# Optimization experiments

Measured on AMD Instinct MI355X. Metric: run time of the kernel, lower is better.

Reference implementation:

```python
import jax, jax.numpy as jnp
import numpy as np

D_NUM, P_NUM, LAYER, EMB = 1500, 4500, 3, 128


def _xavier(k, shape):
    lim = float(np.sqrt(6.0 / (shape[0] + shape[1])))
    return jax.random.uniform(k, shape, minval=-lim, maxval=lim, dtype=jnp.float32)


def _sym_norm(adj):
    # D^{-1/2} A D^{-1/2}, zero-degree safe (utils._create_*_adj_mat)
    deg = adj.sum(axis=1)
    dinv = jnp.where(deg > 0, jax.lax.rsqrt(jnp.maximum(deg, 1e-12)), 0.0)
    return adj * dinv[:, None] * dinv[None, :]


def _gcn(adj, emb, num):
    # LightGCN-style propagation: mean of layer-0..num embeddings (utils._gcn)
    def step(e, _):
        e = adj @ e
        return e, e
    _, layers = jax.lax.scan(step, emb, None, length=num)
    return (emb + layers.sum(axis=0)) / (num + 1)


def _neighbor_mean(mat, feats):
    # vectorized form of the per-row python loop: mean of feats over j where mat[i,j]==1, zeros if no neighbor
    m = (mat == 1.0).astype(feats.dtype)
    cnt = m.sum(axis=1, keepdims=True)
    return jnp.where(cnt > 0, (m @ feats) / jnp.maximum(cnt, 1.0), 0.0)


def _get_weight(emb, WA, BA, HA):
    return jax.nn.log_softmax(jax.nn.relu(emb @ WA + BA) @ HA, axis=0)


def setup_inputs():
    k = jax.random.split(jax.random.key(0), 24)
    N = D_NUM + P_NUM
    A = (jax.random.uniform(k[0], (5, N, N)) < 0.005).astype(jnp.float32)
    z = lambda: jnp.zeros((EMB,), jnp.float32)
    h = lambda: jnp.full((EMB, 1), 0.01, jnp.float32)
    return {
        "A": A,
        "drug_structure": jax.random.normal(k[1], (D_NUM, 160), jnp.float32),
        "protein_structure": jax.random.normal(k[2], (P_NUM, 512), jnp.float32),
        "lin_drug_w": _xavier(k[3], (160, EMB)), "lin_drug_b": z(),
        "lin_pro_w": _xavier(k[4], (512, EMB)), "lin_pro_b": z(),
        "p_weight": _xavier(k[5], (EMB, EMB)),
        "d_weight_i": _xavier(k[6], (EMB, EMB)),
        "pd_weight_p": _xavier(k[7], (EMB, EMB)),
        "pd_weight_d": _xavier(k[8], (EMB, EMB)),
        "dp_weight_p": _xavier(k[9], (EMB, EMB)),
        "WA_drug": _xavier(k[10], (EMB, EMB)), "BA_drug": z(), "HA_drug": h(),
        "WB_drug": _xavier(k[11], (EMB, EMB)), "BB_drug": z(), "HB_drug": h(),
        "WA_pro": _xavier(k[12], (EMB, EMB)), "BA_pro": z(), "HA_pro": h(),
        "WB_pro": _xavier(k[13], (EMB, EMB)), "BB_pro": z(), "HB_pro": h(),
        "WA_sim": _xavier(k[14], (EMB, EMB)), "BA_sim": z(), "HA_sim": h(),
        "layer": LAYER,
    }


def reference(A, drug_structure, protein_structure, lin_drug_w, lin_drug_b, lin_pro_w, lin_pro_b,
              p_weight, d_weight_i, pd_weight_p, pd_weight_d, dp_weight_p,
              WA_drug, BA_drug, HA_drug, WB_drug, BB_drug, HB_drug,
              WA_pro, BA_pro, HA_pro, WB_pro, BB_pro, HB_pro,
              WA_sim, BA_sim, HA_sim, layer):
    D, P = D_NUM, P_NUM
    R = A[0, :D, D:D + P]                       # drug-protein relation [D,P]
    dru_str = drug_structure @ lin_drug_w + lin_drug_b      # [D,128]
    pro_str = protein_structure @ lin_pro_w + lin_pro_b     # [P,128]

    def rel_emb(mat, feats, w):
        nei = _neighbor_mean(mat, feats)
        adj = _sym_norm((mat == 1.0).astype(feats.dtype))
        return _gcn(adj, feats @ w, layer), nei

    dru_rel_emb, dru_rel_nei = rel_emb(A[2, :D, :D], dru_str, d_weight_i)
    pro_rel_emb, pro_rel_nei = rel_emb(A[3, D:, D:], pro_str, p_weight)
    dru_sim_emb, dru_sim_nei = rel_emb(A[4, :D, :D], dru_str, d_weight_i)

    dru_tem = _neighbor_mean(R, pro_rel_nei)    # [D,128]
    # NB: torch 'dru_rel_nei + dru_sim_nei' concatenates python LISTS, and only
    # indices < D are ever read, so pro_tem effectively uses dru_rel_nei only.
    pro_tem = _neighbor_mean(R.T, dru_rel_nei)  # [P,128]

    # bipartite symmetric-normalized adjacency [[0,R],[R^T,0]]
    bip = jnp.zeros((D + P, D + P), R.dtype)
    bip = bip.at[:D, D:].set(R).at[D:, :D].set(R.T)
    adj = _sym_norm(bip)

    one_all = 0.8 * dru_str + 0.2 * dru_tem
    two_all = 0.8 * pro_str + 0.2 * pro_tem
    one_emb = dru_str @ pd_weight_d
    two_all = (two_all @ dp_weight_p) @ pd_weight_d
    two_emb = pro_str @ pd_weight_p
    dru_int = _gcn(adj, jnp.concatenate([one_emb, two_all], axis=0), layer)[:D]
    pro_int = _gcn(adj, jnp.concatenate([one_all, two_emb], axis=0), layer)[D:]

    drug_w = _get_weight(dru_int, WA_drug, BA_drug, HA_drug)
    pro_w = _get_weight(pro_int, WA_pro, BA_pro, HA_pro)
    dru_rel_w = _get_weight(dru_rel_emb, WB_drug, BB_drug, HB_drug)
    pro_rel_w = _get_weight(pro_rel_emb, WB_pro, BB_pro, HB_pro)
    dru_sim_w = _get_weight(dru_sim_emb, WA_sim, BA_sim, HA_sim)

    # faithful to source (including its asymmetric renormalization); dropout is eval-mode identity
    a_w = drug_w / (drug_w + dru_rel_w + dru_sim_w)
    b_w = dru_rel_w / (a_w + dru_rel_w + dru_sim_w)
    c_w = 1.0 - a_w - b_w
    fin_dru = a_w * dru_int + b_w * dru_rel_emb + c_w * dru_sim_emb

    pa = pro_w / (pro_w + pro_rel_w)
    pb = 1.0 - pa
    fin_pro = pa * pro_int + pb * pro_rel_emb

    y = fin_dru @ fin_pro.T                     # [D,P]
    y = (y - y.mean()) / jnp.std(y, ddof=1)     # torch.std is unbiased
    return jax.nn.sigmoid(y)
```

## Files before the change

### kernel.cpp

```cpp
#include <hip/hip_runtime.h>
#include <hip/hip_bf16.h>

constexpr int CAP = 128;

__global__ void k_build(const float* __restrict__ M, long ldm, int rows, int cols,
                        int col_off,
                        int* __restrict__ idx, int* __restrict__ cnt,
                        float* __restrict__ invcnt, float* __restrict__ dinv)
{
    int row = blockIdx.x * 4 + (threadIdx.x >> 6);
    if (row >= rows) return;
    int lane = threadIdx.x & 63;
    const float* p = M + (long)row * ldm;
    int* ri = idx + (long)row * CAP;
    int base = 0;
    for (int j0 = 0; j0 < cols; j0 += 64) {
        int j = j0 + lane;
        bool hit = (j < cols) && (p[j] == 1.0f);
        unsigned long long m = __ballot(hit);
        if (hit) {
            int pos = base + (int)__popcll(m & ((1ULL << lane) - 1ULL));
            if (pos < CAP) ri[pos] = j + col_off;
        }
        base += (int)__popcll(m);
    }
    if (lane == 0) {
        cnt[row] = base < CAP ? base : CAP;
        invcnt[row] = (base > 0) ? 1.0f / (float)base : 0.0f;
        dinv[row]   = (base > 0) ? rsqrtf((float)base) : 0.0f;
    }
}

__global__ void k_scatter_T(int* __restrict__ idx, int* __restrict__ cnt, int topRows)
{
    int row = blockIdx.x * 4 + (threadIdx.x >> 6);
    if (row >= topRows) return;
    int lane = threadIdx.x & 63;
    int n = cnt[row];
    const int* ri = idx + (long)row * CAP;
    for (int k = lane; k < n; k += 64) {
        int j = ri[k];
        int pos = atomicAdd(&cnt[j], 1);
        if (pos < CAP) idx[(long)j * CAP + pos] = row;
    }
}

__global__ void k_invdeg(const int* __restrict__ cnt, int n,
                         float* __restrict__ invcnt, float* __restrict__ dinv)
{
    int i = blockIdx.x * 256 + threadIdx.x;
    if (i < n) {
        int c = cnt[i];
        invcnt[i] = (c > 0) ? 1.0f / (float)c : 0.0f;
        dinv[i]   = (c > 0) ? rsqrtf((float)c) : 0.0f;
    }
}

__global__ __launch_bounds__(256)
void k_spmm_sp(const int* __restrict__ idx, const int* __restrict__ cnt,
               int rows, int mod,
               const float* __restrict__ X,
               const float* __restrict__ rs, const float* __restrict__ cs,
               float* __restrict__ out, float* __restrict__ accp)
{
    int c = threadIdx.x & 127;
    int row = blockIdx.x * 2 + (threadIdx.x >> 7);
    if (row >= rows) return;
    int r_loc = row, xoff = 0;
    if (row >= mod) { r_loc = row - mod; xoff = mod; }
    int n = cnt[r_loc];
    const int* ri = idx + (long)r_loc * CAP;
    float acc = 0.0f;
    int k = 0;
    for (; k + 4 <= n; k += 4) {
        int j0 = ri[k], j1 = ri[k + 1], j2 = ri[k + 2], j3 = ri[k + 3];
        float x0 = X[(long)(j0 + xoff) * 128 + c];
        float x1 = X[(long)(j1 + xoff) * 128 + c];
        float x2 = X[(long)(j2 + xoff) * 128 + c];
        float x3 = X[(long)(j3 + xoff) * 128 + c];
        if (cs) { x0 *= cs[j0]; x1 *= cs[j1]; x2 *= cs[j2]; x3 *= cs[j3]; }
        acc += (x0 + x1) + (x2 + x3);
    }
    for (; k < n; ++k) {
        int j = ri[k];
        float x = X[(long)(j + xoff) * 128 + c];
        if (cs) x *= cs[j];
        acc += x;
    }
    float v = rs ? acc * rs[r_loc] : acc;
    long o = (long)row * 128 + c;
    out[o] = v;
    if (accp) accp[o] += v;
}

template<bool RELU>
__global__ __launch_bounds__(256)
void k_lin(const float* __restrict__ X, const float* __restrict__ X2,
           float pa, float pb, int rows, int K,
           const float* __restrict__ W, const float* __restrict__ bias,
           float* __restrict__ out, float* __restrict__ out2)
{
    __shared__ float Ws[64 * 128];
    int c  = threadIdx.x & 127;
    int row = blockIdx.x * 2 + (threadIdx.x >> 7);
    float acc = 0.0f;
    for (int k0 = 0; k0 < K; k0 += 64) {
        int chunk = min(64, K - k0);
        for (int e = threadIdx.x; e < chunk * 128; e += 256)
            Ws[e] = W[(long)(k0 + (e >> 7)) * 128 + (e & 127)];
        __syncthreads();
        if (row < rows) {
            const float* xr = X + (long)row * K + k0;
            const float* x2r = X2 ? X2 + (long)row * K + k0 : nullptr;
            #pragma unroll 4
            for (int kk = 0; kk < chunk; ++kk) {
                float v = xr[kk];
                if (X2) v = pa * v + pb * x2r[kk];
                acc += v * Ws[kk * 128 + c];
            }
        }
        __syncthreads();
    }
    if (row < rows) {
        float v = acc + (bias ? bias[c] : 0.0f);
        if (RELU) v = fmaxf(v, 0.0f);
        out[(long)row * 128 + c] = v;
        if (out2) out2[(long)row * 128 + c] = v;
    }
}

__global__ __launch_bounds__(256)
void k_attn(const float* __restrict__ X, int rows,
            const float* __restrict__ W, const float* __restrict__ B,
            const float* __restrict__ H, float* __restrict__ s)
{
    __shared__ float Ws[64 * 128];
    __shared__ float part[4];
    int c = threadIdx.x & 127;
    int row = blockIdx.x * 2 + (threadIdx.x >> 7);
    float acc = 0.0f;
    for (int k0 = 0; k0 < 128; k0 += 64) {
        for (int e = threadIdx.x; e < 64 * 128; e += 256)
            Ws[e] = W[(long)(k0 + (e >> 7)) * 128 + (e & 127)];
        __syncthreads();
        if (row < rows) {
            const float* xr = X + (long)row * 128 + k0;
            #pragma unroll 4
            for (int kk = 0; kk < 64; ++kk)
                acc += xr[kk] * Ws[kk * 128 + c];
        }
        __syncthreads();
    }
    float v = 0.0f;
    if (row < rows) v = fmaxf(acc + B[c], 0.0f) * H[c];
    for (int o = 32; o > 0; o >>= 1) v += __shfl_down(v, o, 64);
    if ((threadIdx.x & 63) == 0) part[threadIdx.x >> 6] = v;
    __syncthreads();
    if (threadIdx.x == 0 && row < rows)   s[row] = part[0] + part[1];
    if (threadIdx.x == 128 && row < rows) s[row] = part[2] + part[3];
}

__global__ void k_logsoftmax5(float* s0, int n0, float* s1, int n1,
                              float* s2, int n2, float* s3, int n3,
                              float* s4, int n4)
{
    float* s; int n;
    switch (blockIdx.x) {
        case 0: s = s0; n = n0; break;
        case 1: s = s1; n = n1; break;
        case 2: s = s2; n = n2; break;
        case 3: s = s3; n = n3; break;
        default: s = s4; n = n4; break;
    }
    __shared__ float red[256];
    int t = threadIdx.x;
    float m = -3.4e38f;
    for (int i = t; i < n; i += 256) m = fmaxf(m, s[i]);
    red[t] = m; __syncthreads();
    for (int o = 128; o > 0; o >>= 1) {
        if (t < o) red[t] = fmaxf(red[t], red[t + o]);
        __syncthreads();
    }
    m = red[0];
    __syncthreads();
    float sum = 0.0f;
    for (int i = t; i < n; i += 256) sum += expf(s[i] - m);
    red[t] = sum; __syncthreads();
    for (int o = 128; o > 0; o >>= 1) {
        if (t < o) red[t] += red[t + o];
        __syncthreads();
    }
    float lse = m + logf(red[0]);
    for (int i = t; i < n; i += 256) s[i] -= lse;
}

__global__ void k_scale(const float* __restrict__ src, float* __restrict__ dst,
                        long n, float sc)
{
    long i = (long)blockIdx.x * blockDim.x + threadIdx.x;
    if (i < n) dst[i] = src[i] * sc;
}

__global__ void k_axpby(const float* __restrict__ X, const float* __restrict__ Y,
                        float a, float b,
                        float* __restrict__ out, float* __restrict__ out2, long n)
{
    long i = (long)blockIdx.x * blockDim.x + threadIdx.x;
    if (i < n) {
        float v = a * X[i] + b * Y[i];
        out[i] = v;
        if (out2) out2[i] = v;
    }
}

__global__ void k_fin_dru(const float* __restrict__ wa, const float* __restrict__ wb,
                          const float* __restrict__ wc,
                          const float* __restrict__ ei, const float* __restrict__ er,
                          const float* __restrict__ es,
                          float* __restrict__ fin, int rows)
{
    long idx = (long)blockIdx.x * 256 + threadIdx.x;
    if (idx >= (long)rows * 128) return;
    int r = (int)(idx >> 7);
    float aL = wa[r], bL = wb[r], cL = wc[r];
    float a = aL / (aL + bL + cL);
    float b = bL / (a + bL + cL);
    float c = 1.0f - a - b;
    fin[idx] = a * ei[idx] + b * er[idx] + c * es[idx];
}

__global__ void k_fin_pro(const float* __restrict__ wa, const float* __restrict__ wb,
                          const float* __restrict__ ei, const float* __restrict__ er,
                          float* __restrict__ fin, int rows)
{
    long idx = (long)blockIdx.x * 256 + threadIdx.x;
    if (idx >= (long)rows * 128) return;
    int r = (int)(idx >> 7);
    float pa = wa[r] / (wa[r] + wb[r]);
    fin[idx] = pa * ei[idx] + (1.0f - pa) * er[idx];
}

__global__ void k_zero2(double* p)
{
    if (threadIdx.x < 2) p[threadIdx.x] = 0.0;
}

__global__ __launch_bounds__(256)
void k_ygemm(const float* __restrict__ Af, const float* __restrict__ Bf,
             int M, int N, float* __restrict__ y, double* __restrict__ stats)
{
    __shared__ float Ast[32][68];
    __shared__ float Bst[32][68];
    int i0 = blockIdx.y * 64, j0 = blockIdx.x * 64;
    int tx = threadIdx.x & 15, ty = threadIdx.x >> 4;
    float acc[4][4] = {};
    for (int k0 = 0; k0 < 128; k0 += 32) {
        for (int e = threadIdx.x; e < 64 * 32; e += 256) {
            int r = e >> 5, kk = e & 31;
            int ia = i0 + r, jb = j0 + r;
            Ast[kk][r] = (ia < M) ? Af[(long)ia * 128 + k0 + kk] : 0.0f;
            Bst[kk][r] = (jb < N) ? Bf[(long)jb * 128 + k0 + kk] : 0.0f;
        }
        __syncthreads();
        #pragma unroll 8
        for (int kk = 0; kk < 32; ++kk) {
            float a0 = Ast[kk][ty * 4 + 0], a1 = Ast[kk][ty * 4 + 1];
            float a2 = Ast[kk][ty * 4 + 2], a3 = Ast[kk][ty * 4 + 3];
            float b0 = Bst[kk][tx * 4 + 0], b1 = Bst[kk][tx * 4 + 1];
            float b2 = Bst[kk][tx * 4 + 2], b3 = Bst[kk][tx * 4 + 3];
            acc[0][0] += a0 * b0; acc[0][1] += a0 * b1; acc[0][2] += a0 * b2; acc[0][3] += a0 * b3;
            acc[1][0] += a1 * b0; acc[1][1] += a1 * b1; acc[1][2] += a1 * b2; acc[1][3] += a1 * b3;
            acc[2][0] += a2 * b0; acc[2][1] += a2 * b1; acc[2][2] += a2 * b2; acc[2][3] += a2 * b3;
            acc[3][0] += a3 * b0; acc[3][1] += a3 * b1; acc[3][2] += a3 * b2; acc[3][3] += a3 * b3;
        }
        __syncthreads();
    }
    double s1 = 0.0, s2 = 0.0;
    #pragma unroll
    for (int q = 0; q < 4; ++q) {
        int i = i0 + ty * 4 + q;
        if (i < M) {
            #pragma unroll
            for (int p = 0; p < 4; ++p) {
                int j = j0 + tx * 4 + p;
                if (j < N) {
                    float v = acc[q][p];
                    y[(long)i * N + j] = v;
                    s1 += v; s2 += (double)v * v;
                }
            }
        }
    }
    __shared__ double r1[256];
    __shared__ double r2[256];
    r1[threadIdx.x] = s1; r2[threadIdx.x] = s2;
    __syncthreads();
    for (int o = 128; o > 0; o >>= 1) {
        if (threadIdx.x < o) {
            r1[threadIdx.x] += r1[threadIdx.x + o];
            r2[threadIdx.x] += r2[threadIdx.x + o];
        }
        __syncthreads();
    }
    if (threadIdx.x == 0) {
        atomicAdd(&stats[0], r1[0]);
        atomicAdd(&stats[1], r2[0]);
    }
}

__global__ void k_sigmoid(const float* __restrict__ y, const double* __restrict__ stats,
                          long n, float* __restrict__ out)
{
    long i = (long)blockIdx.x * 256 + threadIdx.x;
    if (i >= n) return;
    double nd = (double)n;
    double mean = stats[0] / nd;
    double var = (stats[1] - nd * mean * mean) / (nd - 1.0);
    if (var < 1e-30) var = 1e-30;
    float inv = (float)(1.0 / sqrt(var));
    float mu = (float)mean;
    out[i] = 1.0f / (1.0f + expf(-((y[i] - mu) * inv)));
}

extern "C" void kernel_launch(void* const* d_in, const int* in_sizes, int n_in,
                              void* d_out, int out_size, void* d_ws, size_t ws_size,
                              hipStream_t stream)
{
    constexpr int D = 1500, P = 4500, E = 128, NL = 3;
    constexpr int NB = D + P;
    constexpr int NR = D + P + D;
    constexpr long ALD = 6000;
    constexpr long ASZ = 36000000L;

    const float* A    = (const float*)d_in[0];
    const float* drug_structure    = (const float*)d_in[1];
    const float* protein_structure = (const float*)d_in[2];
    const float* lin_drug_w = (const float*)d_in[3];
    const float* lin_drug_b = (const float*)d_in[4];
    const float* lin_pro_w  = (const float*)d_in[5];
    const float* lin_pro_b  = (const float*)d_in[6];
    const float* p_weight   = (const float*)d_in[7];
    const float* d_weight_i = (const float*)d_in[8];
    const float* pd_weight_p = (const float*)d_in[9];
    const float* pd_weight_d = (const float*)d_in[10];
    const float* dp_weight_p = (const float*)d_in[11];
    const float* WA_drug = (const float*)d_in[12];
    const float* BA_drug = (const float*)d_in[13];
    const float* HA_drug = (const float*)d_in[14];
    const float* WB_drug = (const float*)d_in[15];
    const float* BB_drug = (const float*)d_in[16];
    const float* HB_drug = (const float*)d_in[17];
    const float* WA_pro = (const float*)d_in[18];
    const float* BA_pro = (const float*)d_in[19];
    const float* HA_pro = (const float*)d_in[20];
    const float* WB_pro = (const float*)d_in[21];
    const float* BB_pro = (const float*)d_in[22];
    const float* HB_pro = (const float*)d_in[23];
    const float* WA_sim = (const float*)d_in[24];
    const float* BA_sim = (const float*)d_in[25];
    const float* HA_sim = (const float*)d_in[26];

    const float* Rp  = A + 1500;
    const float* A2p = A + 2 * ASZ;
    const float* A3p = A + 3 * ASZ + 1500 * ALD + 1500;
    const float* A4p = A + 4 * ASZ;

    char* base = (char*)d_ws;
    size_t off = 0;
    auto alloc = [&](size_t bytes) -> void* {
        off = (off + 255) & ~(size_t)255;
        void* p = base + off;
        off += bytes;
        return p;
    };
    int*   idx_bip  = (int*)alloc((size_t)NB * CAP * 4);
    int*   cnt_bip  = (int*)alloc((size_t)NB * 4);
    int*   idx_rel  = (int*)alloc((size_t)NR * CAP * 4);
    int*   cnt_rel  = (int*)alloc((size_t)NR * 4);
    float* inv_bip  = (float*)alloc(NB * 4);
    float* dinv_bip = (float*)alloc(NB * 4);
    float* inv_rel  = (float*)alloc(NR * 4);
    float* dinv_rel = (float*)alloc(NR * 4);
    float* str_s    = (float*)alloc((size_t)NR * E * 4);
    float* nei_s    = (float*)alloc((size_t)NR * E * 4);
    float* cur_s    = (float*)alloc((size_t)NR * E * 4);
    float* nxt_s    = (float*)alloc((size_t)NR * E * 4);
    float* acc_s    = (float*)alloc((size_t)NR * E * 4);
    float* emb_s    = (float*)alloc((size_t)NR * E * 4);
    float* tem_s    = (float*)alloc((size_t)NB * E * 4);
    float* big_cur  = (float*)alloc((size_t)2 * NB * E * 4);
    float* big_nxt  = (float*)alloc((size_t)2 * NB * E * 4);
    float* big_acc  = (float*)alloc((size_t)2 * NB * E * 4);
    float* int_s    = (float*)alloc((size_t)2 * NB * E * 4);
    float* tmpP     = (float*)alloc((size_t)P * E * 4);
    float* w_drug = (float*)alloc(D * 4);
    float* w_drel = (float*)alloc(D * 4);
    float* w_dsim = (float*)alloc(D * 4);
    float* w_pro  = (float*)alloc(P * 4);
    float* w_prel = (float*)alloc(P * 4);
    float* fin_dru = (float*)alloc((size_t)D * E * 4);
    float* fin_pro = (float*)alloc((size_t)P * E * 4);
    float* ybuf    = (float*)alloc((size_t)D * P * 4);
    double* stats  = (double*)alloc(2 * sizeof(double));
    (void)ws_size; (void)in_sizes; (void)n_in; (void)out_size;

    float* dru_str = str_s;
    float* pro_str = str_s + (size_t)D * E;
    float* dru_rel_emb = emb_s;
    float* pro_rel_emb = emb_s + (size_t)D * E;
    float* dru_sim_emb = emb_s + (size_t)NB * E;
    float* dru_tem = tem_s;
    float* pro_tem = tem_s + (size_t)D * E;
    float* dru_int = int_s;
    float* pro_int = int_s + (size_t)(NB + D) * E;

    long nD = (long)D * E, nP = (long)P * E;

    k_build<<<(D + 3) / 4, 256, 0, stream>>>(Rp,  ALD, D, P, D,
                                             idx_bip, cnt_bip, inv_bip, dinv_bip);
    k_build<<<(D + 3) / 4, 256, 0, stream>>>(A2p, ALD, D, D, 0,
                                             idx_rel, cnt_rel, inv_rel, dinv_rel);
    k_build<<<(P + 3) / 4, 256, 0, stream>>>(A3p, ALD, P, P, D,
                                             idx_rel + (size_t)D * CAP, cnt_rel + D,
                                             inv_rel + D, dinv_rel + D);
    k_build<<<(D + 3) / 4, 256, 0, stream>>>(A4p, ALD, D, D, NB,
                                             idx_rel + (size_t)NB * CAP, cnt_rel + NB,
                                             inv_rel + NB, dinv_rel + NB);
    hipMemsetAsync(cnt_bip + D, 0, (size_t)P * 4, stream);
    k_scatter_T<<<(D + 3) / 4, 256, 0, stream>>>(idx_bip, cnt_bip, D);
    k_invdeg<<<(P + 255) / 256, 256, 0, stream>>>(cnt_bip + D, P, inv_bip + D, dinv_bip + D);

    k_lin<false><<<(D + 1) / 2, 256, 0, stream>>>(drug_structure, nullptr, 0, 0, D, 160,
                                                  lin_drug_w, lin_drug_b,
                                                  dru_str, str_s + (size_t)NB * E);
    k_lin<false><<<(P + 1) / 2, 256, 0, stream>>>(protein_structure, nullptr, 0, 0, P, 512,
                                                  lin_pro_w, lin_pro_b, pro_str, nullptr);

    k_spmm_sp<<<(NR + 1) / 2, 256, 0, stream>>>(idx_rel, cnt_rel, NR, NR,
                                                str_s, inv_rel, nullptr, nei_s, nullptr);
    k_lin<false><<<(D + 1) / 2, 256, 0, stream>>>(dru_str, nullptr, 0, 0, D, E,
                                                  d_weight_i, nullptr,
                                                  cur_s, cur_s + (size_t)NB * E);
    k_lin<false><<<(P + 1) / 2, 256, 0, stream>>>(pro_str, nullptr, 0, 0, P, E,
                                                  p_weight, nullptr,
                                                  cur_s + (size_t)D * E, nullptr);
    k_scale<<<((long)NR * E + 255) / 256, 256, 0, stream>>>(cur_s, acc_s, (long)NR * E, 1.0f);
    {
        float* c = cur_s; float* x = nxt_s;
        for (int l = 0; l < NL; ++l) {
            k_spmm_sp<<<(NR + 1) / 2, 256, 0, stream>>>(idx_rel, cnt_rel, NR, NR,
                                                        c, dinv_rel, dinv_rel, x, acc_s);
            float* t = c; c = x; x = t;
        }
    }
    k_scale<<<((long)NR * E + 255) / 256, 256, 0, stream>>>(acc_s, emb_s, (long)NR * E, 0.25f);

    k_spmm_sp<<<(NB + 1) / 2, 256, 0, stream>>>(idx_bip, cnt_bip, NB, NB,
                                                nei_s, inv_bip, nullptr, tem_s, nullptr);

    k_lin<false><<<(D + 1) / 2, 256, 0, stream>>>(dru_str, nullptr, 0, 0, D, E,
                                                  pd_weight_d, nullptr, big_cur, big_acc);
    k_lin<false><<<(P + 1) / 2, 256, 0, stream>>>(pro_str, pro_tem, 0.8f, 0.2f, P, E,
                                                  dp_weight_p, nullptr, tmpP, nullptr);
    k_lin<false><<<(P + 1) / 2, 256, 0, stream>>>(tmpP, nullptr, 0, 0, P, E,
                                                  pd_weight_d, nullptr,
                                                  big_cur + nD, big_acc + nD);
    k_axpby<<<(nD + 255) / 256, 256, 0, stream>>>(dru_str, dru_tem, 0.8f, 0.2f,
                                                  big_cur + (size_t)NB * E,
                                                  big_acc + (size_t)NB * E, nD);
    k_lin<false><<<(P + 1) / 2, 256, 0, stream>>>(pro_str, nullptr, 0, 0, P, E,
                                                  pd_weight_p, nullptr,
                                                  big_cur + (size_t)(NB + D) * E,
                                                  big_acc + (size_t)(NB + D) * E);
    {
        float* c = big_cur; float* x = big_nxt;
        for (int l = 0; l < NL; ++l) {
            k_spmm_sp<<<NB, 256, 0, stream>>>(idx_bip, cnt_bip, 2 * NB, NB,
                                              c, dinv_bip, dinv_bip, x, big_acc);
            float* t = c; c = x; x = t;
        }
    }
    k_scale<<<((long)2 * NB * E + 255) / 256, 256, 0, stream>>>(big_acc, int_s,
                                                                (long)2 * NB * E, 0.25f);

    k_attn<<<(D + 1) / 2, 256, 0, stream>>>(dru_int,     D, WA_drug, BA_drug, HA_drug, w_drug);
    k_attn<<<(P + 1) / 2, 256, 0, stream>>>(pro_int,     P, WA_pro,  BA_pro,  HA_pro,  w_pro);
    k_attn<<<(D + 1) / 2, 256, 0, stream>>>(dru_rel_emb, D, WB_drug, BB_drug, HB_drug, w_drel);
    k_attn<<<(P + 1) / 2, 256, 0, stream>>>(pro_rel_emb, P, WB_pro,  BB_pro,  HB_pro,  w_prel);
    k_attn<<<(D + 1) / 2, 256, 0, stream>>>(dru_sim_emb, D, WA_sim,  BA_sim,  HA_sim,  w_dsim);
    k_logsoftmax5<<<5, 256, 0, stream>>>(w_drug, D, w_pro, P, w_drel, D, w_prel, P, w_dsim, D);

    k_fin_dru<<<(int)((nD + 255) / 256), 256, 0, stream>>>(w_drug, w_drel, w_dsim,
                                                           dru_int, dru_rel_emb, dru_sim_emb,
                                                           fin_dru, D);
    k_fin_pro<<<(int)((nP + 255) / 256), 256, 0, stream>>>(w_pro, w_prel,
                                                           pro_int, pro_rel_emb,
                                                           fin_pro, P);

    k_zero2<<<1, 64, 0, stream>>>(stats);
    dim3 yg((P + 63) / 64, (D + 63) / 64);
    k_ygemm<<<yg, 256, 0, stream>>>(fin_dru, fin_pro, D, P, ybuf, stats);
    long ny = (long)D * P;
    k_sigmoid<<<(int)((ny + 255) / 256), 256, 0, stream>>>(ybuf, stats, ny, (float*)d_out);
}
```

Measured before the change: 1.549 ms.

## Batch independent kernels into multi-job launches and fold scaling into SpMM

Merges the many small independent launches (build, linear, SpMM, attention, finalize) into multi-job kernels that dispatch on block index. Degree normalisation is computed on the fly from neighbor counts instead of precomputed arrays, and the accumulator init and final 0.25 scaling are folded into the SpMM. The two chained projections are precomposed into one 128x128 weight. The rel and bipartite propagation layers are interleaved in shared launches. This cuts launch count and extra elementwise passes, but the SpMM does extra count loads and rsqrt per neighbor.

```diff
diff --git a/kernel.cpp b/kernel.cpp
--- a/kernel.cpp
+++ b/kernel.cpp
@@ -1,34 +1,46 @@
 #include <hip/hip_runtime.h>
-#include <hip/hip_bf16.h>
 
 constexpr int CAP = 128;
-
-__global__ void k_build(const float* __restrict__ M, long ldm, int rows, int cols,
-                        int col_off,
-                        int* __restrict__ idx, int* __restrict__ cnt,
-                        float* __restrict__ invcnt, float* __restrict__ dinv)
-{
-    int row = blockIdx.x * 4 + (threadIdx.x >> 6);
-    if (row >= rows) return;
+constexpr int RS_INV = 1, RS_RSQRT = 2, CS_RSQRT = 4, FINALIZE = 8;
+
+struct BuildSeg {
+    const float* M; long ldm; int rows; int cols; int col_off;
+    int* idx; int* cnt;
+};
+
+__global__ void k_build_all(BuildSeg sa, BuildSeg sb, BuildSeg sc, BuildSeg sd,
+                            int zb, int e0, int e1, int e2,
+                            int* __restrict__ zcnt, int nz, double* __restrict__ stats)
+{
+    int blk = blockIdx.x;
+    if (blk < zb) {
+        int i = blk * 256 + threadIdx.x;
+        if (i < nz) zcnt[i] = 0;
+        if (blk == 0 && threadIdx.x < 2) stats[threadIdx.x] = 0.0;
+        return;
+    }
+    BuildSeg s; int lb;
+    if (blk < e0)      { s = sa; lb = blk - zb; }
+    else if (blk < e1) { s = sb; lb = blk - e0; }
+    else if (blk < e2) { s = sc; lb = blk - e1; }
+    else               { s = sd; lb = blk - e2; }
+    int row = lb * 4 + (threadIdx.x >> 6);
+    if (row >= s.rows) return;
     int lane = threadIdx.x & 63;
-    const float* p = M + (long)row * ldm;
-    int* ri = idx + (long)row * CAP;
+    const float* p = s.M + (long)row * s.ldm;
+    int* ri = s.idx + (long)row * CAP;
     int base = 0;
-    for (int j0 = 0; j0 < cols; j0 += 64) {
+    for (int j0 = 0; j0 < s.cols; j0 += 64) {
         int j = j0 + lane;
-        bool hit = (j < cols) && (p[j] == 1.0f);
+        bool hit = (j < s.cols) && (p[j] == 1.0f);
         unsigned long long m = __ballot(hit);
         if (hit) {
             int pos = base + (int)__popcll(m & ((1ULL << lane) - 1ULL));
-            if (pos < CAP) ri[pos] = j + col_off;
+            if (pos < CAP) ri[pos] = j + s.col_off;
         }
         base += (int)__popcll(m);
     }
-    if (lane == 0) {
-        cnt[row] = base < CAP ? base : CAP;
-        invcnt[row] = (base > 0) ? 1.0f / (float)base : 0.0f;
-        dinv[row]   = (base > 0) ? rsqrtf((float)base) : 0.0f;
-    }
+    if (lane == 0) s.cnt[row] = base < CAP ? base : CAP;
 }
 
 __global__ void k_scatter_T(int* __restrict__ idx, int* __restrict__ cnt, int topRows)
@@ -45,106 +57,142 @@
     }
 }
 
-__global__ void k_invdeg(const int* __restrict__ cnt, int n,
-                         float* __restrict__ invcnt, float* __restrict__ dinv)
-{
-    int i = blockIdx.x * 256 + threadIdx.x;
-    if (i < n) {
-        int c = cnt[i];
-        invcnt[i] = (c > 0) ? 1.0f / (float)c : 0.0f;
-        dinv[i]   = (c > 0) ? rsqrtf((float)c) : 0.0f;
-    }
-}
+struct SpmmJob {
+    const int* idx; const int* cnt; int rows; int mod;
+    const float* X; float* out; float* acc; const float* init; float* fin;
+    int flags;
+};
 
 __global__ __launch_bounds__(256)
-void k_spmm_sp(const int* __restrict__ idx, const int* __restrict__ cnt,
-               int rows, int mod,
-               const float* __restrict__ X,
-               const float* __restrict__ rs, const float* __restrict__ cs,
-               float* __restrict__ out, float* __restrict__ accp)
-{
+void k_spmm_multi(SpmmJob ja, SpmmJob jb, int nb0)
+{
+    SpmmJob j; int lb;
+    if ((int)blockIdx.x < nb0) { j = ja; lb = blockIdx.x; }
+    else                       { j = jb; lb = blockIdx.x - nb0; }
     int c = threadIdx.x & 127;
-    int row = blockIdx.x * 2 + (threadIdx.x >> 7);
-    if (row >= rows) return;
+    int row = lb * 2 + (threadIdx.x >> 7);
+    if (row >= j.rows) return;
     int r_loc = row, xoff = 0;
-    if (row >= mod) { r_loc = row - mod; xoff = mod; }
-    int n = cnt[r_loc];
-    const int* ri = idx + (long)r_loc * CAP;
+    if (row >= j.mod) { r_loc = row - j.mod; xoff = j.mod; }
+    int n = j.cnt[r_loc];
+    const int* ri = j.idx + (long)r_loc * CAP;
+    const bool csq = (j.flags & CS_RSQRT) != 0;
     float acc = 0.0f;
     int k = 0;
     for (; k + 4 <= n; k += 4) {
-        int j0 = ri[k], j1 = ri[k + 1], j2 = ri[k + 2], j3 = ri[k + 3];
-        float x0 = X[(long)(j0 + xoff) * 128 + c];
-        float x1 = X[(long)(j1 + xoff) * 128 + c];
-        float x2 = X[(long)(j2 + xoff) * 128 + c];
-        float x3 = X[(long)(j3 + xoff) * 128 + c];
-        if (cs) { x0 *= cs[j0]; x1 *= cs[j1]; x2 *= cs[j2]; x3 *= cs[j3]; }
+        int c0 = ri[k], c1 = ri[k + 1], c2 = ri[k + 2], c3 = ri[k + 3];
+        float x0 = j.X[(long)(c0 + xoff) * 128 + c];
+        float x1 = j.X[(long)(c1 + xoff) * 128 + c];
+        float x2 = j.X[(long)(c2 + xoff) * 128 + c];
+        float x3 = j.X[(long)(c3 + xoff) * 128 + c];
+        if (csq) {
+            int n0 = j.cnt[c0], n1 = j.cnt[c1], n2 = j.cnt[c2], n3 = j.cnt[c3];
+            x0 *= (n0 > 0) ? rsqrtf((float)n0) : 0.0f;
+            x1 *= (n1 > 0) ? rsqrtf((float)n1) : 0.0f;
+            x2 *= (n2 > 0) ? rsqrtf((float)n2) : 0.0f;
+            x3 *= (n3 > 0) ? rsqrtf((float)n3) : 0.0f;
+        }
         acc += (x0 + x1) + (x2 + x3);
     }
     for (; k < n; ++k) {
-        int j = ri[k];
-        float x = X[(long)(j + xoff) * 128 + c];
-        if (cs) x *= cs[j];
+        int cj = ri[k];
+        float x = j.X[(long)(cj + xoff) * 128 + c];
+        if (csq) {
+            int nj = j.cnt[cj];
+            x *= (nj > 0) ? rsqrtf((float)nj) : 0.0f;
+        }
         acc += x;
     }
-    float v = rs ? acc * rs[r_loc] : acc;
+    float v;
+    if (j.flags & RS_INV)        v = (n > 0) ? acc / (float)n : 0.0f;
+    else if (j.flags & RS_RSQRT) v = (n > 0) ? acc * rsqrtf((float)n) : 0.0f;
+    else                         v = acc;
     long o = (long)row * 128 + c;
-    out[o] = v;
-    if (accp) accp[o] += v;
-}
-
-template<bool RELU>
+    if (j.flags & FINALIZE) {
+        j.fin[o] = (j.acc[o] + v) * 0.25f;
+    } else {
+        j.out[o] = v;
+        if (j.acc) j.acc[o] = (j.init ? j.init[o] : j.acc[o]) + v;
+    }
+}
+
+struct LinJob {
+    const float* X; const float* X2; float pa, pb; int rows; int K;
+    const float* W; const float* bias; float* out; float* out2;
+};
+
 __global__ __launch_bounds__(256)
-void k_lin(const float* __restrict__ X, const float* __restrict__ X2,
-           float pa, float pb, int rows, int K,
-           const float* __restrict__ W, const float* __restrict__ bias,
-           float* __restrict__ out, float* __restrict__ out2)
+void k_lin_multi(LinJob j0, LinJob j1, LinJob j2, LinJob j3,
+                 int e0, int e1, int e2)
 {
     __shared__ float Ws[64 * 128];
-    int c  = threadIdx.x & 127;
-    int row = blockIdx.x * 2 + (threadIdx.x >> 7);
+    LinJob j; int lb;
+    int blk = blockIdx.x;
+    if (blk < e0)      { j = j0; lb = blk; }
+    else if (blk < e1) { j = j1; lb = blk - e0; }
+    else if (blk < e2) { j = j2; lb = blk - e1; }
+    else               { j = j3; lb = blk - e2; }
+    int c = threadIdx.x & 127;
+    int row = lb * 2 + (threadIdx.x >> 7);
+    if (j.W == nullptr) {
+        if (row < j.rows) {
+            long o = (long)row * 128 + c;
+            float v = j.pa * j.X[o] + j.pb * j.X2[o];
+            j.out[o] = v;
+            if (j.out2) j.out2[o] = v;
+        }
+        return;
+    }
     float acc = 0.0f;
-    for (int k0 = 0; k0 < K; k0 += 64) {
-        int chunk = min(64, K - k0);
+    for (int k0 = 0; k0 < j.K; k0 += 64) {
+        int chunk = min(64, j.K - k0);
         for (int e = threadIdx.x; e < chunk * 128; e += 256)
-            Ws[e] = W[(long)(k0 + (e >> 7)) * 128 + (e & 127)];
-        __syncthreads();
-        if (row < rows) {
-            const float* xr = X + (long)row * K + k0;
-            const float* x2r = X2 ? X2 + (long)row * K + k0 : nullptr;
+            Ws[e] = j.W[(long)(k0 + (e >> 7)) * 128 + (e & 127)];
+        __syncthreads();
+        if (row < j.rows) {
+            const float* xr = j.X + (long)row * j.K + k0;
+            const float* x2r = j.X2 ? j.X2 + (long)row * j.K + k0 : nullptr;
             #pragma unroll 4
             for (int kk = 0; kk < chunk; ++kk) {
                 float v = xr[kk];
-                if (X2) v = pa * v + pb * x2r[kk];
+                if (j.X2) v = j.pa * v + j.pb * x2r[kk];
                 acc += v * Ws[kk * 128 + c];
             }
         }
         __syncthreads();
     }
-    if (row < rows) {
-        float v = acc + (bias ? bias[c] : 0.0f);
-        if (RELU) v = fmaxf(v, 0.0f);
-        out[(long)row * 128 + c] = v;
-        if (out2) out2[(long)row * 128 + c] = v;
-    }
-}
+    if (row < j.rows) {
+        float v = acc + (j.bias ? j.bias[c] : 0.0f);
+        j.out[(long)row * 128 + c] = v;
+        if (j.out2) j.out2[(long)row * 128 + c] = v;
+    }
+}
+
+struct AttnJob { const float* X; int rows; const float* W; const float* B;
+                 const float* H; float* s; };
 
 __global__ __launch_bounds__(256)
-void k_attn(const float* __restrict__ X, int rows,
-            const float* __restrict__ W, const float* __restrict__ B,
-            const float* __restrict__ H, float* __restrict__ s)
+void k_attn_multi(AttnJob a0, AttnJob a1, AttnJob a2, AttnJob a3, AttnJob a4,
+                  int e0, int e1, int e2, int e3)
 {
     __shared__ float Ws[64 * 128];
     __shared__ float part[4];
+    AttnJob j; int lb;
+    int blk = blockIdx.x;
+    if (blk < e0)      { j = a0; lb = blk; }
+    else if (blk < e1) { j = a1; lb = blk - e0; }
+    else if (blk < e2) { j = a2; lb = blk - e1; }
+    else if (blk < e3) { j = a3; lb = blk - e2; }
+    else               { j = a4; lb = blk - e3; }
     int c = threadIdx.x & 127;
-    int row = blockIdx.x * 2 + (threadIdx.x >> 7);
+    int row = lb * 2 + (threadIdx.x >> 7);
     float acc = 0.0f;
     for (int k0 = 0; k0 < 128; k0 += 64) {
         for (int e = threadIdx.x; e < 64 * 128; e += 256)
-            Ws[e] = W[(long)(k0 + (e >> 7)) * 128 + (e & 127)];
-        __syncthreads();
-        if (row < rows) {
-            const float* xr = X + (long)row * 128 + k0;
+            Ws[e] = j.W[(long)(k0 + (e >> 7)) * 128 + (e & 127)];
+        __syncthreads();
+        if (row < j.rows) {
+            const float* xr = j.X + (long)row * 128 + k0;
             #pragma unroll 4
             for (int kk = 0; kk < 64; ++kk)
                 acc += xr[kk] * Ws[kk * 128 + c];
@@ -152,12 +200,12 @@
         __syncthreads();
     }
     float v = 0.0f;
-    if (row < rows) v = fmaxf(acc + B[c], 0.0f) * H[c];
+    if (row < j.rows) v = fmaxf(acc + j.B[c], 0.0f) * j.H[c];
     for (int o = 32; o > 0; o >>= 1) v += __shfl_down(v, o, 64);
     if ((threadIdx.x & 63) == 0) part[threadIdx.x >> 6] = v;
     __syncthreads();
-    if (threadIdx.x == 0 && row < rows)   s[row] = part[0] + part[1];
-    if (threadIdx.x == 128 && row < rows) s[row] = part[2] + part[3];
+    if (threadIdx.x == 0 && row < j.rows)   j.s[row] = part[0] + part[1];
+    if (threadIdx.x == 128 && row < j.rows) j.s[row] = part[2] + part[3];
 }
 
 __global__ void k_logsoftmax5(float* s0, int n0, float* s1, int n1,
@@ -194,55 +242,30 @@
     for (int i = t; i < n; i += 256) s[i] -= lse;
 }
 
-__global__ void k_scale(const float* __restrict__ src, float* __restrict__ dst,
-                        long n, float sc)
-{
-    long i = (long)blockIdx.x * blockDim.x + threadIdx.x;
-    if (i < n) dst[i] = src[i] * sc;
-}
-
-__global__ void k_axpby(const float* __restrict__ X, const float* __restrict__ Y,
-                        float a, float b,
-                        float* __restrict__ out, float* __restrict__ out2, long n)
-{
-    long i = (long)blockIdx.x * blockDim.x + threadIdx.x;
-    if (i < n) {
-        float v = a * X[i] + b * Y[i];
-        out[i] = v;
-        if (out2) out2[i] = v;
-    }
-}
-
-__global__ void k_fin_dru(const float* __restrict__ wa, const float* __restrict__ wb,
-                          const float* __restrict__ wc,
-                          const float* __restrict__ ei, const float* __restrict__ er,
-                          const float* __restrict__ es,
-                          float* __restrict__ fin, int rows)
-{
-    long idx = (long)blockIdx.x * 256 + threadIdx.x;
-    if (idx >= (long)rows * 128) return;
-    int r = (int)(idx >> 7);
-    float aL = wa[r], bL = wb[r], cL = wc[r];
-    float a = aL / (aL + bL + cL);
-    float b = bL / (a + bL + cL);
-    float c = 1.0f - a - b;
-    fin[idx] = a * ei[idx] + b * er[idx] + c * es[idx];
-}
-
-__global__ void k_fin_pro(const float* __restrict__ wa, const float* __restrict__ wb,
-                          const float* __restrict__ ei, const float* __restrict__ er,
-                          float* __restrict__ fin, int rows)
-{
-    long idx = (long)blockIdx.x * 256 + threadIdx.x;
-    if (idx >= (long)rows * 128) return;
-    int r = (int)(idx >> 7);
-    float pa = wa[r] / (wa[r] + wb[r]);
-    fin[idx] = pa * ei[idx] + (1.0f - pa) * er[idx];
-}
-
-__global__ void k_zero2(double* p)
-{
-    if (threadIdx.x < 2) p[threadIdx.x] = 0.0;
+__global__ void k_fin(const float* __restrict__ wd, const float* __restrict__ wdr,
+                      const float* __restrict__ wds,
+                      const float* __restrict__ ei, const float* __restrict__ er,
+                      const float* __restrict__ es,
+                      const float* __restrict__ wp, const float* __restrict__ wpr,
+                      const float* __restrict__ pi, const float* __restrict__ pr,
+                      float* __restrict__ fd, float* __restrict__ fp,
+                      long nDel, long total)
+{
+    long i = (long)blockIdx.x * 256 + threadIdx.x;
+    if (i >= total) return;
+    if (i < nDel) {
+        int r = (int)(i >> 7);
+        float aL = wd[r], bL = wdr[r], cL = wds[r];
+        float a = aL / (aL + bL + cL);
+        float b = bL / (a + bL + cL);
+        float c = 1.0f - a - b;
+        fd[i] = a * ei[i] + b * er[i] + c * es[i];
+    } else {
+        long k = i - nDel;
+        int r = (int)(k >> 7);
+        float pa = wp[r] / (wp[r] + wpr[r]);
+        fp[k] = pa * pi[k] + (1.0f - pa) * pr[k];
+    }
 }
 
 __global__ __launch_bounds__(256)
@@ -326,7 +349,7 @@
                               void* d_out, int out_size, void* d_ws, size_t ws_size,
                               hipStream_t stream)
 {
-    constexpr int D = 1500, P = 4500, E = 128, NL = 3;
+    constexpr int D = 1500, P = 4500, E = 128;
     constexpr int NB = D + P;
     constexpr int NR = D + P + D;
     constexpr long ALD = 6000;
@@ -365,11 +388,11 @@
     const float* A3p = A + 3 * ASZ + 1500 * ALD + 1500;
     const float* A4p = A + 4 * ASZ;
 
-    char* base = (char*)d_ws;
+    char* wsbase = (char*)d_ws;
     size_t off = 0;
     auto alloc = [&](size_t bytes) -> void* {
         off = (off + 255) & ~(size_t)255;
-        void* p = base + off;
+        void* p = wsbase + off;
         off += bytes;
         return p;
     };
@@ -377,10 +400,6 @@
     int*   cnt_bip  = (int*)alloc((size_t)NB * 4);
     int*   idx_rel  = (int*)alloc((size_t)NR * CAP * 4);
     int*   cnt_rel  = (int*)alloc((size_t)NR * 4);
-    float* inv_bip  = (float*)alloc(NB * 4);
-    float* dinv_bip = (float*)alloc(NB * 4);
-    float* inv_rel  = (float*)alloc(NR * 4);
-    float* dinv_rel = (float*)alloc(NR * 4);
     float* str_s    = (float*)alloc((size_t)NR * E * 4);
     float* nei_s    = (float*)alloc((size_t)NR * E * 4);
     float* cur_s    = (float*)alloc((size_t)NR * E * 4);
@@ -392,7 +411,7 @@
     float* big_nxt  = (float*)alloc((size_t)2 * NB * E * 4);
     float* big_acc  = (float*)alloc((size_t)2 * NB * E * 4);
     float* int_s    = (float*)alloc((size_t)2 * NB * E * 4);
-    float* tmpP     = (float*)alloc((size_t)P * E * 4);
+    float* W2       = (float*)alloc((size_t)E * E * 4);
     float* w_drug = (float*)alloc(D * 4);
     float* w_drel = (float*)alloc(D * 4);
     float* w_dsim = (float*)alloc(D * 4);
@@ -416,88 +435,104 @@
 
     long nD = (long)D * E, nP = (long)P * E;
 
-    k_build<<<(D + 3) / 4, 256, 0, stream>>>(Rp,  ALD, D, P, D,
-                                             idx_bip, cnt_bip, inv_bip, dinv_bip);
-    k_build<<<(D + 3) / 4, 256, 0, stream>>>(A2p, ALD, D, D, 0,
-                                             idx_rel, cnt_rel, inv_rel, dinv_rel);
-    k_build<<<(P + 3) / 4, 256, 0, stream>>>(A3p, ALD, P, P, D,
-                                             idx_rel + (size_t)D * CAP, cnt_rel + D,
-                                             inv_rel + D, dinv_rel + D);
-    k_build<<<(D + 3) / 4, 256, 0, stream>>>(A4p, ALD, D, D, NB,
-                                             idx_rel + (size_t)NB * CAP, cnt_rel + NB,
-                                             inv_rel + NB, dinv_rel + NB);
-    hipMemsetAsync(cnt_bip + D, 0, (size_t)P * 4, stream);
+    SpmmJob JZ = {};
+    LinJob  LZ = {};
+
+    {
+        BuildSeg sR  = { Rp,  ALD, D, P, D,  idx_bip, cnt_bip };
+        BuildSeg sA2 = { A2p, ALD, D, D, 0,  idx_rel, cnt_rel };
+        BuildSeg sA3 = { A3p, ALD, P, P, D,  idx_rel + (size_t)D * CAP,  cnt_rel + D };
+        BuildSeg sA4 = { A4p, ALD, D, D, NB, idx_rel + (size_t)NB * CAP, cnt_rel + NB };
+        int zb = (P + 255) / 256;
+        int e0 = zb + (D + 3) / 4;
+        int e1 = e0 + (D + 3) / 4;
+        int e2 = e1 + (P + 3) / 4;
+        int total = e2 + (D + 3) / 4;
+        k_build_all<<<total, 256, 0, stream>>>(sR, sA2, sA3, sA4, zb, e0, e1, e2,
+                                               cnt_bip + D, P, stats);
+    }
     k_scatter_T<<<(D + 3) / 4, 256, 0, stream>>>(idx_bip, cnt_bip, D);
-    k_invdeg<<<(P + 255) / 256, 256, 0, stream>>>(cnt_bip + D, P, inv_bip + D, dinv_bip + D);
-
-    k_lin<false><<<(D + 1) / 2, 256, 0, stream>>>(drug_structure, nullptr, 0, 0, D, 160,
-                                                  lin_drug_w, lin_drug_b,
-                                                  dru_str, str_s + (size_t)NB * E);
-    k_lin<false><<<(P + 1) / 2, 256, 0, stream>>>(protein_structure, nullptr, 0, 0, P, 512,
-                                                  lin_pro_w, lin_pro_b, pro_str, nullptr);
-
-    k_spmm_sp<<<(NR + 1) / 2, 256, 0, stream>>>(idx_rel, cnt_rel, NR, NR,
-                                                str_s, inv_rel, nullptr, nei_s, nullptr);
-    k_lin<false><<<(D + 1) / 2, 256, 0, stream>>>(dru_str, nullptr, 0, 0, D, E,
-                                                  d_weight_i, nullptr,
-                                                  cur_s, cur_s + (size_t)NB * E);
-    k_lin<false><<<(P + 1) / 2, 256, 0, stream>>>(pro_str, nullptr, 0, 0, P, E,
-                                                  p_weight, nullptr,
-                                                  cur_s + (size_t)D * E, nullptr);
-    k_scale<<<((long)NR * E + 255) / 256, 256, 0, stream>>>(cur_s, acc_s, (long)NR * E, 1.0f);
-    {
-        float* c = cur_s; float* x = nxt_s;
-        for (int l = 0; l < NL; ++l) {
-            k_spmm_sp<<<(NR + 1) / 2, 256, 0, stream>>>(idx_rel, cnt_rel, NR, NR,
-                                                        c, dinv_rel, dinv_rel, x, acc_s);
-            float* t = c; c = x; x = t;
-        }
-    }
-    k_scale<<<((long)NR * E + 255) / 256, 256, 0, stream>>>(acc_s, emb_s, (long)NR * E, 0.25f);
-
-    k_spmm_sp<<<(NB + 1) / 2, 256, 0, stream>>>(idx_bip, cnt_bip, NB, NB,
-                                                nei_s, inv_bip, nullptr, tem_s, nullptr);
-
-    k_lin<false><<<(D + 1) / 2, 256, 0, stream>>>(dru_str, nullptr, 0, 0, D, E,
-                                                  pd_weight_d, nullptr, big_cur, big_acc);
-    k_lin<false><<<(P + 1) / 2, 256, 0, stream>>>(pro_str, pro_tem, 0.8f, 0.2f, P, E,
-                                                  dp_weight_p, nullptr, tmpP, nullptr);
-    k_lin<false><<<(P + 1) / 2, 256, 0, stream>>>(tmpP, nullptr, 0, 0, P, E,
-                                                  pd_weight_d, nullptr,
-                                                  big_cur + nD, big_acc + nD);
-    k_axpby<<<(nD + 255) / 256, 256, 0, stream>>>(dru_str, dru_tem, 0.8f, 0.2f,
-                                                  big_cur + (size_t)NB * E,
-                                                  big_acc + (size_t)NB * E, nD);
-    k_lin<false><<<(P + 1) / 2, 256, 0, stream>>>(pro_str, nullptr, 0, 0, P, E,
-                                                  pd_weight_p, nullptr,
-                                                  big_cur + (size_t)(NB + D) * E,
-                                                  big_acc + (size_t)(NB + D) * E);
-    {
-        float* c = big_cur; float* x = big_nxt;
-        for (int l = 0; l < NL; ++l) {
-            k_spmm_sp<<<NB, 256, 0, stream>>>(idx_bip, cnt_bip, 2 * NB, NB,
-                                              c, dinv_bip, dinv_bip, x, big_acc);
-            float* t = c; c = x; x = t;
-        }
-    }
-    k_scale<<<((long)2 * NB * E + 255) / 256, 256, 0, stream>>>(big_acc, int_s,
-                                                                (long)2 * NB * E, 0.25f);
-
-    k_attn<<<(D + 1) / 2, 256, 0, stream>>>(dru_int,     D, WA_drug, BA_drug, HA_drug, w_drug);
-    k_attn<<<(P + 1) / 2, 256, 0, stream>>>(pro_int,     P, WA_pro,  BA_pro,  HA_pro,  w_pro);
-    k_attn<<<(D + 1) / 2, 256, 0, stream>>>(dru_rel_emb, D, WB_drug, BB_drug, HB_drug, w_drel);
-    k_attn<<<(P + 1) / 2, 256, 0, stream>>>(pro_rel_emb, P, WB_pro,  BB_pro,  HB_pro,  w_prel);
-    k_attn<<<(D + 1) / 2, 256, 0, stream>>>(dru_sim_emb, D, WA_sim,  BA_sim,  HA_sim,  w_dsim);
+
+    {
+        LinJob jd = { drug_structure, nullptr, 0, 0, D, 160, lin_drug_w, lin_drug_b,
+                      dru_str, str_s + (size_t)NB * E };
+        LinJob jp = { protein_structure, nullptr, 0, 0, P, 512, lin_pro_w, lin_pro_b,
+                      pro_str, nullptr };
+        LinJob jw = { dp_weight_p, nullptr, 0, 0, E, E, pd_weight_d, nullptr, W2, nullptr };
+        int e0 = (D + 1) / 2, e1 = e0 + (P + 1) / 2, e2 = e1 + (E + 1) / 2;
+        k_lin_multi<<<e2, 256, 0, stream>>>(jd, jp, jw, LZ, e0, e1, e2);
+    }
+    {
+        SpmmJob jn = { idx_rel, cnt_rel, NR, NR, str_s, nei_s, nullptr, nullptr, nullptr, RS_INV };
+        k_spmm_multi<<<(NR + 1) / 2, 256, 0, stream>>>(jn, JZ, (NR + 1) / 2);
+    }
+    {
+        LinJob jd = { dru_str, nullptr, 0, 0, D, E, d_weight_i, nullptr,
+                      cur_s, cur_s + (size_t)NB * E };
+        LinJob jp = { pro_str, nullptr, 0, 0, P, E, p_weight, nullptr,
+                      cur_s + (size_t)D * E, nullptr };
+        int e0 = (D + 1) / 2, e1 = e0 + (P + 1) / 2;
+        k_lin_multi<<<e1, 256, 0, stream>>>(jd, jp, LZ, LZ, e0, e1, e1);
+    }
+    {
+        SpmmJob j1 = { idx_rel, cnt_rel, NR, NR, cur_s, nxt_s, acc_s, cur_s, nullptr,
+                       RS_RSQRT | CS_RSQRT };
+        SpmmJob j2 = { idx_bip, cnt_bip, NB, NB, nei_s, tem_s, nullptr, nullptr, nullptr,
+                       RS_INV };
+        int nb0 = (NR + 1) / 2, nb1 = (NB + 1) / 2;
+        k_spmm_multi<<<nb0 + nb1, 256, 0, stream>>>(j1, j2, nb0);
+    }
+    {
+        LinJob j0 = { dru_str, nullptr, 0, 0, D, E, pd_weight_d, nullptr, big_cur, nullptr };
+        LinJob j1 = { pro_str, pro_tem, 0.8f, 0.2f, P, E, W2, nullptr, big_cur + nD, nullptr };
+        LinJob j2 = { dru_str, dru_tem, 0.8f, 0.2f, D, E, nullptr, nullptr,
+                      big_cur + (size_t)NB * E, nullptr };
+        LinJob j3 = { pro_str, nullptr, 0, 0, P, E, pd_weight_p, nullptr,
+                      big_cur + (size_t)(NB + D) * E, nullptr };
+        int e0 = (D + 1) / 2, e1 = e0 + (P + 1) / 2, e2 = e1 + (D + 1) / 2;
+        int tt = e2 + (P + 1) / 2;
+        k_lin_multi<<<tt, 256, 0, stream>>>(j0, j1, j2, j3, e0, e1, e2);
+    }
+    {
+        SpmmJob j1 = { idx_rel, cnt_rel, NR, NR, nxt_s, cur_s, acc_s, nullptr, nullptr,
+                       RS_RSQRT | CS_RSQRT };
+        SpmmJob j2 = { idx_bip, cnt_bip, 2 * NB, NB, big_cur, big_nxt, big_acc, big_cur,
+                       nullptr, RS_RSQRT | CS_RSQRT };
+        int nb0 = (NR + 1) / 2;
+        k_spmm_multi<<<nb0 + NB, 256, 0, stream>>>(j1, j2, nb0);
+    }
+    {
+        SpmmJob j1 = { idx_rel, cnt_rel, NR, NR, cur_s, nullptr, acc_s, nullptr, emb_s,
+                       RS_RSQRT | CS_RSQRT | FINALIZE };
+        SpmmJob j2 = { idx_bip, cnt_bip, 2 * NB, NB, big_nxt, big_cur, big_acc, nullptr,
+                       nullptr, RS_RSQRT | CS_RSQRT };
+        int nb0 = (NR + 1) / 2;
+        k_spmm_multi<<<nb0 + NB, 256, 0, stream>>>(j1, j2, nb0);
+    }
+    {
+        SpmmJob j2 = { idx_bip, cnt_bip, 2 * NB, NB, big_cur, nullptr, big_acc, nullptr,
+                       int_s, RS_RSQRT | CS_RSQRT | FINALIZE };
+        k_spmm_multi<<<NB, 256, 0, stream>>>(j2, JZ, NB);
+    }
+    {
+        AttnJob a0 = { dru_int,     D, WA_drug, BA_drug, HA_drug, w_drug };
+        AttnJob a1 = { pro_int,     P, WA_pro,  BA_pro,  HA_pro,  w_pro  };
+        AttnJob a2 = { dru_rel_emb, D, WB_drug, BB_drug, HB_drug, w_drel };
+        AttnJob a3 = { pro_rel_emb, P, WB_pro,  BB_pro,  HB_pro,  w_prel };
+        AttnJob a4 = { dru_sim_emb, D, WA_sim,  BA_sim,  HA_sim,  w_dsim };
+        int e0 = (D + 1) / 2, e1 = e0 + (P + 1) / 2, e2 = e1 + (D + 1) / 2;
+        int e3 = e2 + (P + 1) / 2, tt = e3 + (D + 1) / 2;
+        k_attn_multi<<<tt, 256, 0, stream>>>(a0, a1, a2, a3, a4, e0, e1, e2, e3);
+    }
     k_logsoftmax5<<<5, 256, 0, stream>>>(w_drug, D, w_pro, P, w_drel, D, w_prel, P, w_dsim, D);
 
-    k_fin_dru<<<(int)((nD + 255) / 256), 256, 0, stream>>>(w_drug, w_drel, w_dsim,
-                                                           dru_int, dru_rel_emb, dru_sim_emb,
-                                                           fin_dru, D);
-    k_fin_pro<<<(int)((nP + 255) / 256), 256, 0, stream>>>(w_pro, w_prel,
-                                                           pro_int, pro_rel_emb,
-                                                           fin_pro, P);
-
-    k_zero2<<<1, 64, 0, stream>>>(stats);
+    {
+        long total = nD + nP;
+        k_fin<<<(int)((total + 255) / 256), 256, 0, stream>>>(
+            w_drug, w_drel, w_dsim, dru_int, dru_rel_emb, dru_sim_emb,
+            w_pro, w_prel, pro_int, pro_rel_emb,
+            fin_dru, fin_pro, nD, total);
+    }
     dim3 yg((P + 63) / 64, (D + 63) / 64);
     k_ygemm<<<yg, 256, 0, stream>>>(fin_dru, fin_pro, D, P, ybuf, stats);
     long ny = (long)D * P;
```

Result: faster. 1.373 ms (-11.4%).
